# Performance work log

Measured on AMD Instinct MI355X. Metric: run time of the kernel, lower is better.

## Reference

```python
import jax, jax.numpy as jnp
import numpy as np

K = 64
M = 256
V = 5000

def setup_inputs() -> dict:
    key = jax.random.key(0)
    ks = jax.random.split(key, 8)
    feat_x = jax.random.normal(ks[0], (1, V, M), dtype=jnp.float32)
    feat_y = jax.random.normal(ks[1], (1, V, M), dtype=jnp.float32)
    evals_x = jnp.sort(jax.random.uniform(ks[2], (1, K), dtype=jnp.float32))
    evals_y = jnp.sort(jax.random.uniform(ks[3], (1, K), dtype=jnp.float32))
    evecs_trans_x = jax.random.normal(ks[4], (1, K, V), dtype=jnp.float32) / np.sqrt(V)
    evecs_trans_y = jax.random.normal(ks[5], (1, K, V), dtype=jnp.float32) / np.sqrt(V)
    eye = jnp.eye(K, dtype=jnp.float32)
    sqrtMk_x = (eye + 0.05 * jax.random.normal(ks[6], (K, K), dtype=jnp.float32))[None]
    sqrtMk_y = (eye + 0.05 * jax.random.normal(ks[7], (K, K), dtype=jnp.float32))[None]
    return {"feat_x": feat_x, "feat_y": feat_y, "evals_x": evals_x, "evals_y": evals_y,
            "evecs_trans_x": evecs_trans_x, "evecs_trans_y": evecs_trans_y,
            "sqrtMk_x": sqrtMk_x, "sqrtMk_y": sqrtMk_y}

LMBDA = 0.001

def _fmap(fx, fy, ex, ey, tx, ty, sx, sy):
    # squeeze batch dim of 1 (as in torch .squeeze())
    fx, fy = fx[0], fy[0]            # [V, m]
    ex, ey = ex[0], ey[0]            # [k]
    tx, ty = tx[0], ty[0]            # [k, V]
    sx, sy = sx[0], sy[0]            # [k, k]
    A = tx @ fx                      # [k, m] spectral coeffs of feat_x
    B = sy @ (ty @ fy)               # adapt_feature=True: premultiply by sqrtMk_y
    k, m = A.shape
    vec_B = B.T.reshape(m * k, 1)
    At_Ik = jnp.kron(A.T, sy)        # [m*k, k*k] (adapt_feature -> Ik = sqrtMk_y)
    first = At_Ik.T @ At_Ik          # [k^2, k^2]
    # adapt_mask=True branch
    inv_sx = jnp.linalg.inv(sx)
    lx = jnp.diag(ex)
    ly = jnp.diag(ey)
    lx_Ik = jnp.kron(lx @ inv_sx, sy)
    Ik_ly = jnp.kron(inv_sx, sy @ ly)
    Delta = lx_Ik - Ik_ly
    second = Delta.T @ Delta
    rhs = At_Ik.T @ vec_B
    op = first + LMBDA * second
    C = jnp.linalg.solve(op, rhs)
    return C.reshape(k, k).T[None]   # [1, k, k]

def reference(feat_x, feat_y, evals_x, evals_y, evecs_trans_x, evecs_trans_y, sqrtMk_x, sqrtMk_y):
    # bidirectional=False -> only Cxy (Cyx is None in the torch module)
    return _fmap(feat_x, feat_y, evals_x, evals_y, evecs_trans_x, evecs_trans_y, sqrtMk_x, sqrtMk_y)
```

## Files before the change

kernel.cpp:

```cpp
#include <hip/hip_runtime.h>

#define LMBDA 0.001f
#define NS_SY 4
#define NS_G  5
#define NS_SX 5
#define OUTER 3
#define LDP 68

#define WS_A    0
#define WS_FY   16384
#define WS_G1   32768
#define WS_FYAT 36864
#define WS_T1   40960
#define WS_R2   45056
#define WS_R4   49152
#define WS_C    53248
#define WS_FLAGS 57344

#define FMA4(ar, xs, b) { ar[0]=fmaf((xs),(b).x,ar[0]); ar[1]=fmaf((xs),(b).y,ar[1]); \
                          ar[2]=fmaf((xs),(b).z,ar[2]); ar[3]=fmaf((xs),(b).w,ar[3]); }

template<int SA, int SB>
__device__ __forceinline__ void mm64(const float* __restrict__ A,
                                     const float* __restrict__ B,
                                     int ti, int tj, float a[4][4]) {
    #pragma unroll 4
    for (int k = 0; k < 64; k += 4) {
        float4 av0 = *(const float4*)&A[(4 * ti + 0) * SA + k];
        float4 av1 = *(const float4*)&A[(4 * ti + 1) * SA + k];
        float4 av2 = *(const float4*)&A[(4 * ti + 2) * SA + k];
        float4 av3 = *(const float4*)&A[(4 * ti + 3) * SA + k];
        float4 b0 = *(const float4*)&B[(k + 0) * SB + 4 * tj];
        float4 b1 = *(const float4*)&B[(k + 1) * SB + 4 * tj];
        float4 b2 = *(const float4*)&B[(k + 2) * SB + 4 * tj];
        float4 b3 = *(const float4*)&B[(k + 3) * SB + 4 * tj];
        FMA4(a[0], av0.x, b0); FMA4(a[0], av0.y, b1); FMA4(a[0], av0.z, b2); FMA4(a[0], av0.w, b3);
        FMA4(a[1], av1.x, b0); FMA4(a[1], av1.y, b1); FMA4(a[1], av1.z, b2); FMA4(a[1], av1.w, b3);
        FMA4(a[2], av2.x, b0); FMA4(a[2], av2.y, b1); FMA4(a[2], av2.z, b2); FMA4(a[2], av2.w, b3);
        FMA4(a[3], av3.x, b0); FMA4(a[3], av3.y, b1); FMA4(a[3], av3.z, b2); FMA4(a[3], av3.w, b3);
    }
}

template<int SA, int SB>
__device__ __forceinline__ void mmdot(const float* __restrict__ A,
                                      const float* __restrict__ B,
                                      int ti, int tj, float a[4][4]) {
    #pragma unroll 4
    for (int m = 0; m < 64; m += 4) {
        float4 av[4], bv[4];
        #pragma unroll
        for (int r = 0; r < 4; ++r) av[r] = *(const float4*)&A[(4 * ti + r) * SA + m];
        #pragma unroll
        for (int c = 0; c < 4; ++c) bv[c] = *(const float4*)&B[(4 * tj + c) * SB + m];
        #pragma unroll
        for (int r = 0; r < 4; ++r)
            #pragma unroll
            for (int c = 0; c < 4; ++c)
                a[r][c] += av[r].x * bv[c].x + av[r].y * bv[c].y
                         + av[r].z * bv[c].z + av[r].w * bv[c].w;
    }
}

template<int SM>
__device__ __forceinline__ void ns_invert(const float* sM, float* sX, float* sY,
                                          int iters, int ti, int tj,
                                          int tid, float alpha)
{
    for (int idx = tid; idx < 4096; idx += 256) {
        int i = idx >> 6, j = idx & 63;
        sX[i * LDP + j] = (i == j) ? alpha : 0.f;
    }
    __syncthreads();
    for (int it = 0; it < iters; ++it) {
        float y[4][4] = {};
        mm64<SM, LDP>(sM, sX, ti, tj, y);
        #pragma unroll
        for (int r = 0; r < 4; ++r) {
            float4 v = {y[r][0], y[r][1], y[r][2], y[r][3]};
            *(float4*)&sY[(4 * ti + r) * 64 + 4 * tj] = v;
        }
        __syncthreads();
        float z[4][4] = {};
        mm64<LDP, 64>(sX, sY, ti, tj, z);
        __syncthreads();
        #pragma unroll
        for (int r = 0; r < 4; ++r) {
            float4 xv = *(const float4*)&sX[(4 * ti + r) * LDP + 4 * tj];
            xv.x = 2.f * xv.x - z[r][0];
            xv.y = 2.f * xv.y - z[r][1];
            xv.z = 2.f * xv.z - z[r][2];
            xv.w = 2.f * xv.w - z[r][3];
            *(float4*)&sX[(4 * ti + r) * LDP + 4 * tj] = xv;
        }
        __syncthreads();
    }
}

__device__ __forceinline__ void wait_ge(int* flag, int target, int tid) {
    if (tid == 0) {
        while (__hip_atomic_load(flag, __ATOMIC_ACQUIRE, __HIP_MEMORY_SCOPE_AGENT) < target)
            __builtin_amdgcn_s_sleep(8);
    }
    __syncthreads();
    __threadfence();
}

__device__ __forceinline__ void signal_one(int* flag, int tid) {
    __syncthreads();
    __threadfence();
    if (tid == 0)
        (void)__hip_atomic_fetch_add(flag, 1, __ATOMIC_RELEASE, __HIP_MEMORY_SCOPE_AGENT);
}

__global__ __launch_bounds__(256, 1) void fused_fmnet(
    const float* __restrict__ fx, const float* __restrict__ fy,
    const float* __restrict__ ex, const float* __restrict__ ey,
    const float* __restrict__ tx, const float* __restrict__ ty,
    const float* __restrict__ sx, const float* __restrict__ sy,
    float* __restrict__ ws, float* __restrict__ out)
{
    extern __shared__ __align__(16) float lds[];
    int* flags = (int*)(ws + WS_FLAGS);
    const int tid = threadIdx.x;
    const int ti = tid >> 4, tj = tid & 15;
    const int bid = blockIdx.x;

    if (bid < 216) {
        float* sT = lds;
        float* sF = lds + 4352;
        const int gx = bid & 7, gy = bid >> 3;
        const int mat = gx >> 2;
        const int m0 = (gx & 3) << 6;
        const float* __restrict__ T = mat ? ty : tx;
        const float* __restrict__ F = mat ? fy : fx;
        float* __restrict__ Out = ws + (mat ? WS_FY : WS_A);

        float acc[4][4] = {};
        for (int sc = gy; sc * 64 < 5000; sc += 27) {
            const int v0 = sc << 6;
            int vlen = 5000 - v0; if (vlen > 64) vlen = 64;
            #pragma unroll
            for (int w = 0; w < 4; ++w) {
                const int fidx = tid + (w << 8);
                const int row = fidx >> 4, q = fidx & 15;
                const int vv = q << 2;
                if (vv < vlen) {
                    float4 val = *(const float4*)(T + (size_t)row * 5000 + v0 + vv);
                    sT[(vv + 0) * LDP + row] = val.x;
                    sT[(vv + 1) * LDP + row] = val.y;
                    sT[(vv + 2) * LDP + row] = val.z;
                    sT[(vv + 3) * LDP + row] = val.w;
                }
                if (row < vlen) {
                    *(float4*)&sF[row * LDP + (q << 2)] =
                        *(const float4*)(F + (size_t)(v0 + row) * 256 + m0 + (q << 2));
                }
            }
            __syncthreads();
            #pragma unroll 4
            for (int v = 0; v < vlen; ++v) {
                float4 av = *(const float4*)&sT[v * LDP + 4 * ti];
                float4 bv = *(const float4*)&sF[v * LDP + 4 * tj];
                FMA4(acc[0], av.x, bv); FMA4(acc[1], av.y, bv);
                FMA4(acc[2], av.z, bv); FMA4(acc[3], av.w, bv);
            }
            __syncthreads();
        }
        #pragma unroll
        for (int r = 0; r < 4; ++r)
            #pragma unroll
            for (int c = 0; c < 4; ++c)
                atomicAdd(&Out[(4 * ti + r) * 256 + m0 + 4 * tj + c], acc[r][c]);
        __syncthreads();
        __threadfence();
        if (tid == 0)
            (void)__hip_atomic_fetch_add(&flags[gx], 1, __ATOMIC_RELEASE, __HIP_MEMORY_SCOPE_AGENT);
    } else if (bid < 220) {
        const int ch = bid - 216;
        wait_ge(&flags[ch], 27, tid);
        float* sA = lds;
        for (int idx = tid; idx < 1024; idx += 256) {
            int i = idx >> 4, m4 = (idx & 15) << 2;
            *(float4*)&sA[i * LDP + m4] =
                *(const float4*)&ws[WS_A + i * 256 + (ch << 6) + m4];
        }
        __syncthreads();
        float a[4][4] = {};
        mmdot<LDP, LDP>(sA, sA, ti, tj, a);
        #pragma unroll
        for (int r = 0; r < 4; ++r)
            #pragma unroll
            for (int c = 0; c < 4; ++c)
                atomicAdd(&ws[WS_G1 + (4 * ti + r) * 64 + 4 * tj + c], a[r][c]);
        __syncthreads();
        __threadfence();
        if (tid == 0)
            (void)__hip_atomic_fetch_add(&flags[8], 1, __ATOMIC_RELEASE, __HIP_MEMORY_SCOPE_AGENT);
    } else if (bid < 224) {
        const int ch = bid - 220;
        wait_ge(&flags[ch], 27, tid);
        wait_ge(&flags[4 + ch], 27, tid);
        float* sFy = lds;
        float* sAx = lds + 4352;
        for (int idx = tid; idx < 1024; idx += 256) {
            int i = idx >> 4, m4 = (idx & 15) << 2;
            *(float4*)&sFy[i * LDP + m4] = *(const float4*)&ws[WS_FY + i * 256 + (ch << 6) + m4];
            *(float4*)&sAx[i * LDP + m4] = *(const float4*)&ws[WS_A  + i * 256 + (ch << 6) + m4];
        }
        __syncthreads();
        float a[4][4] = {};
        mmdot<LDP, LDP>(sFy, sAx, ti, tj, a);
        #pragma unroll
        for (int r = 0; r < 4; ++r)
            #pragma unroll
            for (int c = 0; c < 4; ++c)
                atomicAdd(&ws[WS_FYAT + (4 * ti + r) * 64 + 4 * tj + c], a[r][c]);
        signal_one(&flags[9], tid);
    } else if (bid == 224) {
        float* sSy = lds;
        float* sXx = lds + 4352;
        float* sYy = lds + 8704;
        float* sH  = lds + 12800;
        float* sV  = lds + 16896;
        for (int idx = tid; idx < 1024; idx += 256) {
            int i = idx >> 4, j4 = (idx & 15) << 2;
            *(float4*)&sSy[i * LDP + j4] = *(const float4*)&sy[i * 64 + j4];
        }
        if (tid < 64) sV[tid] = ey[tid];
        __syncthreads();
        {
            float h[4][4] = {};
            for (int k = 0; k < 64; ++k) {
                float4 av = *(const float4*)&sSy[k * LDP + 4 * ti];
                float4 bv = *(const float4*)&sSy[k * LDP + 4 * tj];
                FMA4(h[0], av.x, bv); FMA4(h[1], av.y, bv);
                FMA4(h[2], av.z, bv); FMA4(h[3], av.w, bv);
            }
            #pragma unroll
            for (int r = 0; r < 4; ++r) {
                float4 v = {h[r][0], h[r][1], h[r][2], h[r][3]};
                *(float4*)&sH[(4 * ti + r) * 64 + 4 * tj] = v;
            }
        }
        __syncthreads();
        ns_invert<LDP>(sSy, sXx, sYy, NS_SY, ti, tj, tid, 1.0f);
        {
            float h[4][4] = {};
            mmdot<LDP, LDP>(sXx, sXx, ti, tj, h);
            __syncthreads();
            #pragma unroll
            for (int r = 0; r < 4; ++r) {
                float4 v = {h[r][0], h[r][1], h[r][2], h[r][3]};
                *(float4*)&sSy[(4 * ti + r) * LDP + 4 * tj] = v;
            }
        }
        __syncthreads();
        {
            float a[4][4] = {};
            #pragma unroll 4
            for (int k = 0; k < 64; k += 4) {
                float4 av[4];
                #pragma unroll
                for (int r = 0; r < 4; ++r) av[r] = *(const float4*)&sSy[(4 * ti + r) * LDP + k];
                #pragma unroll
                for (int q = 0; q < 4; ++q) {
                    float e = sV[k + q];
                    float4 bv = *(const float4*)&sH[(k + q) * 64 + 4 * tj];
                    bv.x *= e; bv.y *= e; bv.z *= e; bv.w *= e;
                    float xq[4] = {av[0].x, av[1].x, av[2].x, av[3].x};
                    if (q == 1) { xq[0]=av[0].y; xq[1]=av[1].y; xq[2]=av[2].y; xq[3]=av[3].y; }
                    if (q == 2) { xq[0]=av[0].z; xq[1]=av[1].z; xq[2]=av[2].z; xq[3]=av[3].z; }
                    if (q == 3) { xq[0]=av[0].w; xq[1]=av[1].w; xq[2]=av[2].w; xq[3]=av[3].w; }
                    #pragma unroll
                    for (int r = 0; r < 4; ++r) FMA4(a[r], xq[r], bv);
                }
            }
            #pragma unroll
            for (int r = 0; r < 4; ++r) {
                float4 v = {a[r][0], a[r][1], a[r][2], a[r][3]};
                *(float4*)&ws[WS_C + (4 * ti + r) * 64 + 4 * tj] = v;
            }
        }
        signal_one(&flags[9], tid);
    } else if (bid == 225) {
        float* sM = lds;
        float* sX = lds + 4352;
        float* sY = lds + 8704;
        float* sV = lds + 12800;
        for (int idx = tid; idx < 1024; idx += 256) {
            int i = idx >> 4, j4 = (idx & 15) << 2;
            *(float4*)&sM[i * LDP + j4] = *(const float4*)&sx[i * 64 + j4];
        }
        if (tid < 64) sV[tid] = ex[tid];
        __syncthreads();
        ns_invert<LDP>(sM, sX, sY, NS_SX, ti, tj, tid, 1.0f);
        float aR2[4][4] = {}, aR4[4][4] = {}, aT1[4][4] = {};
        for (int k = 0; k < 64; ++k) {
            float e = sV[k], e2 = e * e;
            float4 av = *(const float4*)&sX[k * LDP + 4 * ti];
            float4 bv = *(const float4*)&sX[k * LDP + 4 * tj];
            float avv[4] = {av.x, av.y, av.z, av.w};
            #pragma unroll
            for (int r = 0; r < 4; ++r) {
                FMA4(aR4[r], avv[r], bv);
                float ea = e * avv[r];
                FMA4(aR2[r], ea, bv);
                float e2a = e2 * avv[r];
                FMA4(aT1[r], e2a, bv);
            }
        }
        #pragma unroll
        for (int r = 0; r < 4; ++r) {
            int o = (4 * ti + r) * 64 + 4 * tj;
            float4 v2 = {aR2[r][0], aR2[r][1], aR2[r][2], aR2[r][3]};
            float4 v4 = {aR4[r][0], aR4[r][1], aR4[r][2], aR4[r][3]};
            float4 v1 = {aT1[r][0], aT1[r][1], aT1[r][2], aT1[r][3]};
            *(float4*)&ws[WS_R2 + o] = v2;
            *(float4*)&ws[WS_R4 + o] = v4;
            *(float4*)&ws[WS_T1 + o] = v1;
        }
        signal_one(&flags[9], tid);
    } else {
        float* cM1   = lds;
        float* cR2   = lds + 4096;
        float* cR4   = lds + 8192;
        float* cGinv = lds + 12288;
        float* sE    = lds + 16384;
        float* sX    = lds + 20480;
        float* cC    = lds + 24832;
        float* sW    = lds + 29184;

        wait_ge(&flags[8], 4, tid);
        for (int idx = tid; idx < 1024; idx += 256) {
            int i = idx >> 4, j4 = (idx & 15) << 2;
            *(float4*)&cM1[i * 64 + j4] = *(const float4*)&ws[WS_G1 + i * 64 + j4];
        }
        __syncthreads();
        if (tid < 64) {
            float s = 0.f;
            for (int j4 = 0; j4 < 64; j4 += 4) {
                float4 v = *(const float4*)&cM1[tid * 64 + j4];
                s += v.x * v.x + v.y * v.y + v.z * v.z + v.w * v.w;
            }
            sW[tid] = s;
            sW[64 + tid] = cM1[tid * 64 + tid];
        }
        __syncthreads();
        float f2 = 0.f, tr = 0.f;
        for (int i = 0; i < 64; ++i) { f2 += sW[i]; tr += sW[64 + i]; }
        ns_invert<64>(cM1, sX, sE, NS_G, ti, tj, tid, tr / f2);
        for (int idx = tid; idx < 1024; idx += 256) {
            int i = idx >> 4, j4 = (idx & 15) << 2;
            *(float4*)&cGinv[i * 64 + j4] = *(const float4*)&sX[i * LDP + j4];
        }
        wait_ge(&flags[9], 6, tid);
        for (int idx = tid; idx < 1024; idx += 256) {
            int i = idx >> 4, j4 = (idx & 15) << 2;
            int o = i * 64 + j4;
            float4 gv = *(const float4*)&cM1[o];
            float4 t = *(const float4*)&ws[WS_T1 + o];
            gv.x = fmaf(LMBDA, t.x, gv.x); gv.y = fmaf(LMBDA, t.y, gv.y);
            gv.z = fmaf(LMBDA, t.z, gv.z); gv.w = fmaf(LMBDA, t.w, gv.w);
            *(float4*)&cM1[o] = gv;
            *(float4*)&cR2[o] = *(const float4*)&ws[WS_R2 + o];
            *(float4*)&cR4[o] = *(const float4*)&ws[WS_R4 + o];
            *(float4*)&cC[i * LDP + j4] = *(const float4*)&ws[WS_C + o];
        }
        float4 eyv = *(const float4*)&ey[4 * ti];
        float eyr[4] = {eyv.x, eyv.y, eyv.z, eyv.w};
        float leyr[4];
        #pragma unroll
        for (int r = 0; r < 4; ++r) leyr[r] = LMBDA * eyr[r];

        float fyr[4][4], xreg[4][4];
        #pragma unroll
        for (int r = 0; r < 4; ++r) {
            float4 v = *(const float4*)&ws[WS_FYAT + (4 * ti + r) * 64 + 4 * tj];
            fyr[r][0] = v.x; fyr[r][1] = v.y; fyr[r][2] = v.z; fyr[r][3] = v.w;
            float4 z = {0.f, 0.f, 0.f, 0.f};
            *(float4*)&sX[(4 * ti + r) * LDP + 4 * tj] = z;
            #pragma unroll
            for (int c = 0; c < 4; ++c) xreg[r][c] = 0.f;
        }
        __syncthreads();

        float E1[4][4];
        for (int it = 0; it < OUTER; ++it) {
            {
                float Sm[4][4] = {}, S2[4][4] = {}, S4[4][4] = {};
                #pragma unroll 2
                for (int k = 0; k < 64; k += 4) {
                    float4 av[4];
                    #pragma unroll
                    for (int r = 0; r < 4; ++r)
                        av[r] = *(const float4*)&sX[(4 * ti + r) * LDP + k];
                    #pragma unroll
                    for (int q = 0; q < 4; ++q) {
                        float4 mv = *(const float4*)&cM1[(k + q) * 64 + 4 * tj];
                        float4 qv = *(const float4*)&cR2[(k + q) * 64 + 4 * tj];
                        float4 rv = *(const float4*)&cR4[(k + q) * 64 + 4 * tj];
                        float xq[4] = {av[0].x, av[1].x, av[2].x, av[3].x};
                        if (q == 1) { xq[0]=av[0].y; xq[1]=av[1].y; xq[2]=av[2].y; xq[3]=av[3].y; }
                        if (q == 2) { xq[0]=av[0].z; xq[1]=av[1].z; xq[2]=av[2].z; xq[3]=av[3].z; }
                        if (q == 3) { xq[0]=av[0].w; xq[1]=av[1].w; xq[2]=av[2].w; xq[3]=av[3].w; }
                        #pragma unroll
                        for (int r = 0; r < 4; ++r) {
                            FMA4(Sm[r], xq[r], mv);
                            FMA4(S2[r], xq[r], qv);
                            FMA4(S4[r], xq[r], rv);
                        }
                    }
                }
                #pragma unroll
                for (int r = 0; r < 4; ++r) {
                    float4 e2;
                    e2.x = LMBDA * fmaf(eyr[r], S4[r][0], -S2[r][0]);
                    e2.y = LMBDA * fmaf(eyr[r], S4[r][1], -S2[r][1]);
                    e2.z = LMBDA * fmaf(eyr[r], S4[r][2], -S2[r][2]);
                    e2.w = LMBDA * fmaf(eyr[r], S4[r][3], -S2[r][3]);
                    *(float4*)&sE[(4 * ti + r) * 64 + 4 * tj] = e2;
                    #pragma unroll
                    for (int c = 0; c < 4; ++c)
                        E1[r][c] = fmaf(-leyr[r], S2[r][c], Sm[r][c]);
                }
            }
            __syncthreads();
            {
                float Z[4][4] = {};
                mm64<LDP, 64>(cC, sE, ti, tj, Z);
                #pragma unroll
                for (int r = 0; r < 4; ++r) {
                    float4 w;
                    w.x = fyr[r][0] - E1[r][0] - Z[r][0];
                    w.y = fyr[r][1] - E1[r][1] - Z[r][1];
                    w.z = fyr[r][2] - E1[r][2] - Z[r][2];
                    w.w = fyr[r][3] - E1[r][3] - Z[r][3];
                    *(float4*)&sW[(4 * ti + r) * LDP + 4 * tj] = w;
                }
            }
            __syncthreads();
            {
                float dX[4][4] = {};
                mm64<LDP, 64>(sW, cGinv, ti, tj, dX);
                #pragma unroll
                for (int r = 0; r < 4; ++r) {
                    float4 v;
                    #pragma unroll
                    for (int c = 0; c < 4; ++c) xreg[r][c] += dX[r][c];
                    v.x = xreg[r][0]; v.y = xreg[r][1]; v.z = xreg[r][2]; v.w = xreg[r][3];
                    *(float4*)&sX[(4 * ti + r) * LDP + 4 * tj] = v;
                    if (it == OUTER - 1)
                        *(float4*)&out[(4 * ti + r) * 64 + 4 * tj] = v;
                }
            }
            if (it == OUTER - 1) break;
            __syncthreads();
        }
    }
}

extern "C" void kernel_launch(void* const* d_in, const int* in_sizes, int n_in,
                              void* d_out, int out_size, void* d_ws, size_t ws_size,
                              hipStream_t stream) {
    (void)in_sizes; (void)n_in; (void)out_size; (void)ws_size;
    const float* fx = (const float*)d_in[0];
    const float* fy = (const float*)d_in[1];
    const float* ex = (const float*)d_in[2];
    const float* ey = (const float*)d_in[3];
    const float* tx = (const float*)d_in[4];
    const float* ty = (const float*)d_in[5];
    const float* sx = (const float*)d_in[6];
    const float* sy = (const float*)d_in[7];
    float* ws = (float*)d_ws;
    float* out = (float*)d_out;

    (void)hipFuncSetAttribute((const void*)fused_fmnet,
                              hipFuncAttributeMaxDynamicSharedMemorySize, 134144);

    (void)hipMemsetAsync(d_ws, 0, (size_t)(WS_T1) * sizeof(float), stream);
    (void)hipMemsetAsync((char*)d_ws + (size_t)WS_FLAGS * sizeof(float), 0, 64, stream);
    fused_fmnet<<<227, 256, 134144, stream>>>(fx, fy, ex, ey, tx, ty, sx, sy, ws, out);
}
```

Baseline: 190.4 us.

## Register-prefetch next V-chunk, widen projection grid, and fold first Newton-Schulz step

The projection blocks now load the next 64-vertex chunk of T and F into registers while computing on the current chunk in LDS. This hides global-load latency behind the FMA loop. The split along V grows from 27 to 30 groups, giving 240 projection blocks. That uses more CUs on the mi355x and shortens each block's serial chain, and the downstream block indices and flag counts are shifted to match. Newton-Schulz inversion now starts from the closed-form result of the first iteration, saving one pair of 64x64 matmuls per inversion, at the cost of extra register pressure in the projection loop.

```diff
diff --git a/kernel.cpp b/kernel.cpp
--- a/kernel.cpp
+++ b/kernel.cpp
@@ -6,6 +6,7 @@
 #define NS_SX 5
 #define OUTER 3
 #define LDP 68
+#define GYS 30
 
 #define WS_A    0
 #define WS_FY   16384
@@ -66,12 +67,13 @@
                                           int iters, int ti, int tj,
                                           int tid, float alpha)
 {
+    const float a2 = alpha * alpha;
     for (int idx = tid; idx < 4096; idx += 256) {
         int i = idx >> 6, j = idx & 63;
-        sX[i * LDP + j] = (i == j) ? alpha : 0.f;
+        sX[i * LDP + j] = ((i == j) ? 2.f * alpha : 0.f) - a2 * sM[i * SM + j];
     }
     __syncthreads();
-    for (int it = 0; it < iters; ++it) {
+    for (int it = 1; it < iters; ++it) {
         float y[4][4] = {};
         mm64<SM, LDP>(sM, sX, ti, tj, y);
         #pragma unroll
@@ -125,7 +127,7 @@
     const int ti = tid >> 4, tj = tid & 15;
     const int bid = blockIdx.x;
 
-    if (bid < 216) {
+    if (bid < 240) {
         float* sT = lds;
         float* sF = lds + 4352;
         const int gx = bid & 7, gy = bid >> 3;
@@ -135,28 +137,44 @@
         const float* __restrict__ F = mat ? fy : fx;
         float* __restrict__ Out = ws + (mat ? WS_FY : WS_A);
 
+        float4 tv[4], fv[4];
+        int sc = gy;
+        int vlen = 5000 - (sc << 6); if (vlen > 64) vlen = 64;
+        #pragma unroll
+        for (int w = 0; w < 4; ++w) {
+            const int fidx = tid + (w << 8);
+            const int row = fidx >> 4, q = fidx & 15, vv = q << 2;
+            if (vv < vlen) tv[w] = *(const float4*)(T + (size_t)row * 5000 + (sc << 6) + vv);
+            if (row < vlen) fv[w] = *(const float4*)(F + (size_t)((sc << 6) + row) * 256 + m0 + (q << 2));
+        }
+        #pragma unroll
+        for (int w = 0; w < 4; ++w) {
+            const int fidx = tid + (w << 8);
+            const int row = fidx >> 4, q = fidx & 15, vv = q << 2;
+            if (vv < vlen) {
+                sT[(vv + 0) * LDP + row] = tv[w].x;
+                sT[(vv + 1) * LDP + row] = tv[w].y;
+                sT[(vv + 2) * LDP + row] = tv[w].z;
+                sT[(vv + 3) * LDP + row] = tv[w].w;
+            }
+            if (row < vlen) *(float4*)&sF[row * LDP + (q << 2)] = fv[w];
+        }
+        __syncthreads();
+
         float acc[4][4] = {};
-        for (int sc = gy; sc * 64 < 5000; sc += 27) {
-            const int v0 = sc << 6;
-            int vlen = 5000 - v0; if (vlen > 64) vlen = 64;
-            #pragma unroll
-            for (int w = 0; w < 4; ++w) {
-                const int fidx = tid + (w << 8);
-                const int row = fidx >> 4, q = fidx & 15;
-                const int vv = q << 2;
-                if (vv < vlen) {
-                    float4 val = *(const float4*)(T + (size_t)row * 5000 + v0 + vv);
-                    sT[(vv + 0) * LDP + row] = val.x;
-                    sT[(vv + 1) * LDP + row] = val.y;
-                    sT[(vv + 2) * LDP + row] = val.z;
-                    sT[(vv + 3) * LDP + row] = val.w;
-                }
-                if (row < vlen) {
-                    *(float4*)&sF[row * LDP + (q << 2)] =
-                        *(const float4*)(F + (size_t)(v0 + row) * 256 + m0 + (q << 2));
-                }
-            }
-            __syncthreads();
+        for (;;) {
+            const int nsc = sc + GYS;
+            int nvlen = 5000 - (nsc << 6);
+            if (nvlen > 64) nvlen = 64;
+            if (nvlen > 0) {
+                #pragma unroll
+                for (int w = 0; w < 4; ++w) {
+                    const int fidx = tid + (w << 8);
+                    const int row = fidx >> 4, q = fidx & 15, vv = q << 2;
+                    if (vv < nvlen) tv[w] = *(const float4*)(T + (size_t)row * 5000 + (nsc << 6) + vv);
+                    if (row < nvlen) fv[w] = *(const float4*)(F + (size_t)((nsc << 6) + row) * 256 + m0 + (q << 2));
+                }
+            }
             #pragma unroll 4
             for (int v = 0; v < vlen; ++v) {
                 float4 av = *(const float4*)&sT[v * LDP + 4 * ti];
@@ -164,7 +182,22 @@
                 FMA4(acc[0], av.x, bv); FMA4(acc[1], av.y, bv);
                 FMA4(acc[2], av.z, bv); FMA4(acc[3], av.w, bv);
             }
+            if (nvlen <= 0) break;
             __syncthreads();
+            #pragma unroll
+            for (int w = 0; w < 4; ++w) {
+                const int fidx = tid + (w << 8);
+                const int row = fidx >> 4, q = fidx & 15, vv = q << 2;
+                if (vv < nvlen) {
+                    sT[(vv + 0) * LDP + row] = tv[w].x;
+                    sT[(vv + 1) * LDP + row] = tv[w].y;
+                    sT[(vv + 2) * LDP + row] = tv[w].z;
+                    sT[(vv + 3) * LDP + row] = tv[w].w;
+                }
+                if (row < nvlen) *(float4*)&sF[row * LDP + (q << 2)] = fv[w];
+            }
+            __syncthreads();
+            sc = nsc; vlen = nvlen;
         }
         #pragma unroll
         for (int r = 0; r < 4; ++r)
@@ -175,9 +208,9 @@
         __threadfence();
         if (tid == 0)
             (void)__hip_atomic_fetch_add(&flags[gx], 1, __ATOMIC_RELEASE, __HIP_MEMORY_SCOPE_AGENT);
-    } else if (bid < 220) {
-        const int ch = bid - 216;
-        wait_ge(&flags[ch], 27, tid);
+    } else if (bid < 244) {
+        const int ch = bid - 240;
+        wait_ge(&flags[ch], GYS, tid);
         float* sA = lds;
         for (int idx = tid; idx < 1024; idx += 256) {
             int i = idx >> 4, m4 = (idx & 15) << 2;
@@ -196,10 +229,10 @@
         __threadfence();
         if (tid == 0)
             (void)__hip_atomic_fetch_add(&flags[8], 1, __ATOMIC_RELEASE, __HIP_MEMORY_SCOPE_AGENT);
-    } else if (bid < 224) {
-        const int ch = bid - 220;
-        wait_ge(&flags[ch], 27, tid);
-        wait_ge(&flags[4 + ch], 27, tid);
+    } else if (bid < 248) {
+        const int ch = bid - 244;
+        wait_ge(&flags[ch], GYS, tid);
+        wait_ge(&flags[4 + ch], GYS, tid);
         float* sFy = lds;
         float* sAx = lds + 4352;
         for (int idx = tid; idx < 1024; idx += 256) {
@@ -216,7 +249,7 @@
             for (int c = 0; c < 4; ++c)
                 atomicAdd(&ws[WS_FYAT + (4 * ti + r) * 64 + 4 * tj + c], a[r][c]);
         signal_one(&flags[9], tid);
-    } else if (bid == 224) {
+    } else if (bid == 248) {
         float* sSy = lds;
         float* sXx = lds + 4352;
         float* sYy = lds + 8704;
@@ -282,7 +315,7 @@
             }
         }
         signal_one(&flags[9], tid);
-    } else if (bid == 225) {
+    } else if (bid == 249) {
         float* sM = lds;
         float* sX = lds + 4352;
         float* sY = lds + 8704;
@@ -479,5 +512,5 @@
 
     (void)hipMemsetAsync(d_ws, 0, (size_t)(WS_T1) * sizeof(float), stream);
     (void)hipMemsetAsync((char*)d_ws + (size_t)WS_FLAGS * sizeof(float), 0, 64, stream);
-    fused_fmnet<<<227, 256, 134144, stream>>>(fx, fy, ex, ey, tx, ty, sx, sy, ws, out);
-}
+    fused_fmnet<<<251, 256, 134144, stream>>>(fx, fy, ex, ey, tx, ty, sx, sy, ws, out);
+}
```

Result: faster. 182.1 us (-4.3%).
